# Performance work log

Measured on AMD Instinct MI355X. Metric: run time of the kernel, lower is better.

Reference implementation:

```python
import jax, jax.numpy as jnp
import numpy as np

N = 50000   # num_node
E = 1600000 # edge_size (N * avg_degree 32)
B = 64      # batch, hardcoded via repeat(64,1,1) in the torch module


def setup_inputs() -> dict:
    key = jax.random.key(0)
    k = jax.random.split(key, 8)
    return {
        "t": jax.random.normal(k[0], (1,), dtype=jnp.float32),
        "input": jax.random.normal(k[1], (B, N), dtype=jnp.float32),
        "edge_i": jax.random.randint(k[2], (E,), 0, N, dtype=jnp.int32),
        "edge_j": jax.random.randint(k[3], (E,), 0, N, dtype=jnp.int32),
        "weight_react": jax.random.normal(k[4], (1, E), dtype=jnp.float32) / 10.0,
        "weight_diff": jax.random.normal(k[5], (1, E), dtype=jnp.float32) / 1000.0,
        "bias_reaction": jax.random.normal(k[6], (1, N), dtype=jnp.float32) / 10.0,
        "bias_diffusion": jax.random.normal(k[7], (1, N), dtype=jnp.float32) / 10.0,
    }


def _lap_matvec(x, w, src, dst, n):
    # W[src_e, dst_e] = w_e (duplicates coalesce by sum, as torch sparse_coo_tensor does)
    # L = diag(colsum(W)) - W ; returns x @ L^T applied batched: out[b, v] = (L x[b])[v]
    col = jax.ops.segment_sum(w, dst, num_segments=n)                 # [N] column sums
    msg = jax.ops.segment_sum(w[:, None] * x[:, dst].T, src,
                              num_segments=n)                          # [N, B]
    return col[None, :] * x - msg.T                                   # [B, N]


def reference(t, input, edge_i, edge_j, weight_react, weight_diff,
              bias_reaction, bias_diffusion):
    x = input                                                          # [B, N]
    n = x.shape[1]
    # reaction Laplacian uses edges (i -> j); diffusion uses transposed (j -> i)
    reaction = _lap_matvec(x, weight_react[0], edge_i, edge_j, n) + bias_reaction
    diffusion = _lap_matvec(x, weight_diff[0], edge_j, edge_i, n) + bias_diffusion
    # up and down both True: tanh(reaction) + diffusion + input
    return jnp.tanh(reaction) + diffusion + x
```

## Files before the change

kernel.cpp:

```cpp
#include <hip/hip_runtime.h>
#include <hip/hip_fp16.h>


#define BKT_SHIFT 7
#define BKT_NODES 128
#define RCAP 4608
#define RCAP2 4992
#define CH 4096
#define NBP 512

#define RFL(x) __builtin_amdgcn_readfirstlane(x)

__device__ __forceinline__ unsigned bf16_rne(float f) {
    unsigned u = __float_as_uint(f);
    unsigned rb = (u >> 16) & 1u;
    u += 0x7FFFu + rb;
    return u >> 16;
}
__device__ __forceinline__ float bf16_lo(int y) {
    return __uint_as_float(((unsigned)y) << 16);
}
__device__ __forceinline__ float bf16_hi(int y) {
    return __uint_as_float((unsigned)y & 0xFFFF0000u);
}

__global__ void transpose_kernel(const float* __restrict__ x, __half* __restrict__ xth,
                                 int* __restrict__ gcur, int ngcur, int N) {
    __shared__ float tile[64][65];
    int v0 = blockIdx.x * 64;
    int tx = threadIdx.x;
    int ty = threadIdx.y;
    int flat = blockIdx.x * 1024 + ty * 64 + tx;
    if (flat < ngcur) gcur[flat] = 0;
    if (v0 + tx < N) {
        for (int b = ty; b < 64; b += 16)
            tile[tx][b] = x[b * N + v0 + tx];
    }
    __syncthreads();
    for (int vl = ty; vl < 64; vl += 16) {
        int v = v0 + vl;
        if (v < N)
            xth[(size_t)v * 64 + tx] = __float2half(tile[vl][tx]);
    }
}

__global__ void __launch_bounds__(512) partition_kernel(
        const int* __restrict__ ei, const int* __restrict__ ej,
        const float* __restrict__ wr, const float* __restrict__ wd,
        int* __restrict__ gcur, int2* __restrict__ runs,
        int E, int NB) {
    __shared__ int cnt[2 * NBP];
    __shared__ int base_a[2 * NBP];
    __shared__ int gb[2 * NBP];
    __shared__ int2 buf[2 * CH];

    int tid = threadIdx.x;
    int e0 = blockIdx.x * CH;
    int ch_len = min(CH, E - e0);
    if (ch_len <= 0) return;

    int my_i[8], my_j[8];
    unsigned my_w[8];
    #pragma unroll
    for (int k = 0; k < 8; ++k) {
        int t = tid + k * 512;
        if (t < ch_len) {
            int e = e0 + t;
            my_i[k] = ei[e];
            my_j[k] = ej[e];
            my_w[k] = (bf16_rne(wr[e]) << 16) | bf16_rne(wd[e]);
        } else {
            my_i[k] = -1;
        }
    }

    for (int b = tid; b < 2 * NBP; b += 512) cnt[b] = 0;
    __syncthreads();
    #pragma unroll
    for (int k = 0; k < 8; ++k) {
        if (my_i[k] >= 0) {
            atomicAdd(&cnt[my_i[k] >> BKT_SHIFT], 1);
            atomicAdd(&cnt[NBP + (my_j[k] >> BKT_SHIFT)], 1);
        }
    }
    __syncthreads();
    if (tid < 64) {
        int carry = 0;
        #pragma unroll
        for (int c = 0; c < (2 * NBP) / 64; ++c) {
            int idx = c * 64 + tid;
            int val = cnt[idx];
            int scan = val;
            for (int off = 1; off < 64; off <<= 1) {
                int n = __shfl_up(scan, off, 64);
                if (tid >= off) scan += n;
            }
            int excl = scan - val + carry;
            base_a[idx] = excl;
            cnt[idx] = excl;
            carry += __shfl(scan, 63, 64);
        }
    }
    __syncthreads();
    #pragma unroll
    for (int k = 0; k < 8; ++k) {
        if (my_i[k] >= 0) {
            int i = my_i[k], j = my_j[k];
            unsigned wv = my_w[k];
            int b0 = i >> BKT_SHIFT;
            int p0 = atomicAdd(&cnt[b0], 1);
            buf[p0] = make_int2((int)(((unsigned)b0 << 23) | ((unsigned)(i & 127) << 16) | (unsigned)j),
                                (int)wv);
            int b1 = j >> BKT_SHIFT;
            int p1 = atomicAdd(&cnt[NBP + b1], 1);
            buf[p1] = make_int2((int)(((unsigned)b1 << 23) | ((unsigned)(j & 127) << 16) | (unsigned)i),
                                (int)((wv << 16) | (wv >> 16)));
        }
    }
    __syncthreads();
    for (int cb = tid; cb < 2 * NBP; cb += 512) {
        int n = cnt[cb] - base_a[cb];
        if (n > 0) {
            int side = cb >> 9;
            int bkt = cb & (NBP - 1);
            gb[cb] = atomicAdd(&gcur[side * NB + bkt], n);
        }
    }
    __syncthreads();
    int total = 2 * ch_len;
    for (int t = tid; t < total; t += 512) {
        int2 p = buf[t];
        int side = (t >= ch_len) ? 1 : 0;
        int bkt = ((unsigned)p.x >> 23) & 0x1FF;
        int cb = side * NBP + bkt;
        int rank = gb[cb] + (t - base_a[cb]);
        if (rank < RCAP)
            runs[((size_t)(side * NB + bkt)) * RCAP + rank] = p;
    }
}

__global__ void __launch_bounds__(512) sortgather_kernel(
        const int* __restrict__ gcur, const int2* __restrict__ runs,
        const __half* __restrict__ xth,
        __half* __restrict__ msg, float* __restrict__ colsum,
        int NB, int N) {
    __shared__ int cnt[BKT_NODES];
    __shared__ int cur[BKT_NODES];
    __shared__ int pb[BKT_NODES];
    __shared__ float csum[BKT_NODES];
    __shared__ int src_c[RCAP];
    __shared__ unsigned char dlb[RCAP];
    __shared__ int dst[RCAP2];

    int sb = blockIdx.x;
    int side = (sb >= NB) ? 1 : 0;
    int b = sb - side * NB;
    int v0 = b << BKT_SHIFT;
    int len = min(gcur[sb], RCAP);
    size_t roff = (size_t)sb * RCAP;
    int tid = threadIdx.x;

    if (tid < BKT_NODES) { cnt[tid] = 0; csum[tid] = 0.f; }
    __syncthreads();
    for (int k = tid; k < len; k += 512) {
        int2 p = runs[roff + k];
        int dl = ((unsigned)p.x >> 16) & 0x7F;
        src_c[k] = (int)(((unsigned)p.y & 0xFFFF0000u) | ((unsigned)p.x & 0xFFFFu));
        dlb[k] = (unsigned char)dl;
        atomicAdd(&cnt[dl], 1);
        atomicAdd(&csum[dl], bf16_lo(p.y));
    }
    __syncthreads();
    if (tid < 64) {
        int carry = 0;
        #pragma unroll
        for (int c = 0; c < BKT_NODES / 64; ++c) {
            int idx = c * 64 + tid;
            int val = (cnt[idx] + 3) & ~3;
            int scan = val;
            for (int off = 1; off < 64; off <<= 1) {
                int n = __shfl_up(scan, off, 64);
                if (tid >= off) scan += n;
            }
            int excl = scan - val + carry;
            pb[idx] = excl;
            cur[idx] = excl;
            carry += __shfl(scan, 63, 64);
        }
    }
    __syncthreads();
    if (tid < BKT_NODES) {
        int pc = (cnt[tid] + 3) & ~3;
        for (int t = cnt[tid]; t < pc; ++t) dst[pb[tid] + t] = 0;
    }
    __syncthreads();
    for (int k = tid; k < len; k += 512) {
        int dl = dlb[k];
        int pos = atomicAdd(&cur[dl], 1);
        dst[pos] = src_c[k];
    }
    __syncthreads();

    int lane = tid & 63;
    int wid = tid >> 6;
    for (int t = 0; t < BKT_NODES / 8; ++t) {
        int dl = wid * (BKT_NODES / 8) + t;
        int v = v0 + dl;
        if (v >= N) continue;
        int base = pb[dl];
        int n = cnt[dl];
        int nq = (n + 3) >> 2;
        const int4* quads = (const int4*)(dst + base);
        float acc = 0.f;
        int q = 0;
        for (; q + 2 <= nq; q += 2) {
            int4 qa = quads[q];
            int4 qb = quads[q + 1];
            int p0 = RFL(qa.x), p1 = RFL(qa.y), p2 = RFL(qa.z), p3 = RFL(qa.w);
            int p4 = RFL(qb.x), p5 = RFL(qb.y), p6 = RFL(qb.z), p7 = RFL(qb.w);
            float x0 = __half2float(xth[((size_t)(p0 & 0xFFFF) << 6) + lane]);
            float x1 = __half2float(xth[((size_t)(p1 & 0xFFFF) << 6) + lane]);
            float x2 = __half2float(xth[((size_t)(p2 & 0xFFFF) << 6) + lane]);
            float x3 = __half2float(xth[((size_t)(p3 & 0xFFFF) << 6) + lane]);
            float x4 = __half2float(xth[((size_t)(p4 & 0xFFFF) << 6) + lane]);
            float x5 = __half2float(xth[((size_t)(p5 & 0xFFFF) << 6) + lane]);
            float x6 = __half2float(xth[((size_t)(p6 & 0xFFFF) << 6) + lane]);
            float x7 = __half2float(xth[((size_t)(p7 & 0xFFFF) << 6) + lane]);
            acc = fmaf(bf16_hi(p0), x0, acc);
            acc = fmaf(bf16_hi(p1), x1, acc);
            acc = fmaf(bf16_hi(p2), x2, acc);
            acc = fmaf(bf16_hi(p3), x3, acc);
            acc = fmaf(bf16_hi(p4), x4, acc);
            acc = fmaf(bf16_hi(p5), x5, acc);
            acc = fmaf(bf16_hi(p6), x6, acc);
            acc = fmaf(bf16_hi(p7), x7, acc);
        }
        if (q < nq) {
            int4 qa = quads[q];
            int p0 = RFL(qa.x), p1 = RFL(qa.y), p2 = RFL(qa.z), p3 = RFL(qa.w);
            float x0 = __half2float(xth[((size_t)(p0 & 0xFFFF) << 6) + lane]);
            float x1 = __half2float(xth[((size_t)(p1 & 0xFFFF) << 6) + lane]);
            float x2 = __half2float(xth[((size_t)(p2 & 0xFFFF) << 6) + lane]);
            float x3 = __half2float(xth[((size_t)(p3 & 0xFFFF) << 6) + lane]);
            acc = fmaf(bf16_hi(p0), x0, acc);
            acc = fmaf(bf16_hi(p1), x1, acc);
            acc = fmaf(bf16_hi(p2), x2, acc);
            acc = fmaf(bf16_hi(p3), x3, acc);
        }
        msg[((size_t)side * N + v) * 64 + lane] = __float2half(acc);
        if (lane == 0)
            colsum[(size_t)side * N + v] = csum[dl];
    }
}

__global__ void final_kernel(const float* __restrict__ x,
                             const __half* __restrict__ msg,
                             const float* __restrict__ colsum,
                             const float* __restrict__ br, const float* __restrict__ bd,
                             float* __restrict__ out, int N) {
    __shared__ float tr[64][65];
    __shared__ float td[64][65];
    int v0 = blockIdx.x * 64;
    int tx = threadIdx.x;
    int ty = threadIdx.y;
    for (int vl = ty; vl < 64; vl += 16) {
        int v = v0 + vl;
        if (v < N) {
            tr[vl][tx] = __half2float(msg[(size_t)v * 64 + tx]);
            td[vl][tx] = __half2float(msg[((size_t)N + v) * 64 + tx]);
        }
    }
    __syncthreads();
    int v = v0 + tx;
    if (v < N) {
        float cold = colsum[v];
        float colr = colsum[(size_t)N + v];
        float brv = br[v], bdv = bd[v];
        for (int b = ty; b < 64; b += 16) {
            float xv = x[b * N + v];
            float r = colr * xv - tr[tx][b] + brv;
            float d = cold * xv - td[tx][b] + bdv;
            out[b * N + v] = tanhf(r) + d + xv;
        }
    }
}

extern "C" void kernel_launch(void* const* d_in, const int* in_sizes, int n_in,
                              void* d_out, int out_size, void* d_ws, size_t ws_size,
                              hipStream_t stream) {
    const float* x  = (const float*)d_in[1];
    const int*   ei = (const int*)d_in[2];
    const int*   ej = (const int*)d_in[3];
    const float* wr = (const float*)d_in[4];
    const float* wd = (const float*)d_in[5];
    const float* br = (const float*)d_in[6];
    const float* bd = (const float*)d_in[7];
    float* out = (float*)d_out;

    int E = in_sizes[2];
    int N = in_sizes[6];
    int NB = (N + BKT_NODES - 1) >> BKT_SHIFT;
    (void)out_size; (void)ws_size; (void)n_in;

    char* w = (char*)d_ws;
    __half* xth = (__half*)w;    w += (size_t)N * 64 * 2;
    __half* msg = (__half*)w;    w += (size_t)2 * N * 64 * 2;
    float* colsum = (float*)w;   w += (size_t)2 * N * 4;
    int* gcur   = (int*)w;       w += (size_t)2 * NB * 4;
    w = (char*)(((uintptr_t)w + 15) & ~(uintptr_t)15);
    int2* runs  = (int2*)w;

    dim3 tb(64, 16);
    int ntiles = (N + 63) / 64;
    transpose_kernel<<<ntiles, tb, 0, stream>>>(x, xth, gcur, 2 * NB, N);

    int nchunks = (E + CH - 1) / CH;
    partition_kernel<<<nchunks, 512, 0, stream>>>(ei, ej, wr, wd, gcur, runs, E, NB);

    sortgather_kernel<<<2 * NB, 512, 0, stream>>>(gcur, runs, xth, msg, colsum, NB, N);

    final_kernel<<<ntiles, tb, 0, stream>>>(x, msg, colsum, br, bd, out, N);
}
```

Before: 229.7 us.

## Split half-precision x into two 32-batch planes and gather two edges per wavefront

The transposed half-precision input is stored as two planes of 32 batch columns instead of one 64-wide row per node. The gather kernel makes two passes, one per plane. In each pass the two half-waves handle alternate edges and are combined with a cross-lane shuffle, so each gathered row is 64 bytes and the per-pass working set is halved for cache locality. Both partition and sortgather are also raised to 1024 threads per block, which may affect occupancy and adds an extra block barrier per pass.

```diff
diff --git a/kernel.cpp b/kernel.cpp
--- a/kernel.cpp
+++ b/kernel.cpp
@@ -24,7 +24,7 @@
     return __uint_as_float((unsigned)y & 0xFFFF0000u);
 }
 
-__global__ void transpose_kernel(const float* __restrict__ x, __half* __restrict__ xth,
+__global__ void transpose_kernel(const float* __restrict__ x, __half* __restrict__ xh,
                                  int* __restrict__ gcur, int ngcur, int N) {
     __shared__ float tile[64][65];
     int v0 = blockIdx.x * 64;
@@ -37,14 +37,16 @@
             tile[tx][b] = x[b * N + v0 + tx];
     }
     __syncthreads();
+    int pass = tx >> 5;
+    int halfl = tx & 31;
     for (int vl = ty; vl < 64; vl += 16) {
         int v = v0 + vl;
         if (v < N)
-            xth[(size_t)v * 64 + tx] = __float2half(tile[vl][tx]);
-    }
-}
-
-__global__ void __launch_bounds__(512) partition_kernel(
+            xh[((size_t)pass * N + v) * 32 + halfl] = __float2half(tile[vl][tx]);
+    }
+}
+
+__global__ void __launch_bounds__(1024) partition_kernel(
         const int* __restrict__ ei, const int* __restrict__ ej,
         const float* __restrict__ wr, const float* __restrict__ wd,
         int* __restrict__ gcur, int2* __restrict__ runs,
@@ -59,11 +61,11 @@
     int ch_len = min(CH, E - e0);
     if (ch_len <= 0) return;
 
-    int my_i[8], my_j[8];
-    unsigned my_w[8];
+    int my_i[4], my_j[4];
+    unsigned my_w[4];
     #pragma unroll
-    for (int k = 0; k < 8; ++k) {
-        int t = tid + k * 512;
+    for (int k = 0; k < 4; ++k) {
+        int t = tid + k * 1024;
         if (t < ch_len) {
             int e = e0 + t;
             my_i[k] = ei[e];
@@ -74,10 +76,10 @@
         }
     }
 
-    for (int b = tid; b < 2 * NBP; b += 512) cnt[b] = 0;
+    if (tid < 2 * NBP) cnt[tid] = 0;
     __syncthreads();
     #pragma unroll
-    for (int k = 0; k < 8; ++k) {
+    for (int k = 0; k < 4; ++k) {
         if (my_i[k] >= 0) {
             atomicAdd(&cnt[my_i[k] >> BKT_SHIFT], 1);
             atomicAdd(&cnt[NBP + (my_j[k] >> BKT_SHIFT)], 1);
@@ -103,7 +105,7 @@
     }
     __syncthreads();
     #pragma unroll
-    for (int k = 0; k < 8; ++k) {
+    for (int k = 0; k < 4; ++k) {
         if (my_i[k] >= 0) {
             int i = my_i[k], j = my_j[k];
             unsigned wv = my_w[k];
@@ -118,17 +120,17 @@
         }
     }
     __syncthreads();
-    for (int cb = tid; cb < 2 * NBP; cb += 512) {
-        int n = cnt[cb] - base_a[cb];
+    if (tid < 2 * NBP) {
+        int n = cnt[tid] - base_a[tid];
         if (n > 0) {
-            int side = cb >> 9;
-            int bkt = cb & (NBP - 1);
-            gb[cb] = atomicAdd(&gcur[side * NB + bkt], n);
+            int side = tid >> 9;
+            int bkt = tid & (NBP - 1);
+            gb[tid] = atomicAdd(&gcur[side * NB + bkt], n);
         }
     }
     __syncthreads();
     int total = 2 * ch_len;
-    for (int t = tid; t < total; t += 512) {
+    for (int t = tid; t < total; t += 1024) {
         int2 p = buf[t];
         int side = (t >= ch_len) ? 1 : 0;
         int bkt = ((unsigned)p.x >> 23) & 0x1FF;
@@ -139,9 +141,17 @@
     }
 }
 
-__global__ void __launch_bounds__(512) sortgather_kernel(
+__device__ __forceinline__ void pair_acc(int pA, int pB, const __half* __restrict__ xp,
+                                         int halfl, bool hi, float& acc) {
+    int o = hi ? (pB & 0xFFFF) : (pA & 0xFFFF);
+    float w = hi ? bf16_hi(pB) : bf16_hi(pA);
+    float xv = __half2float(xp[((size_t)o << 5) + halfl]);
+    acc = fmaf(w, xv, acc);
+}
+
+__global__ void __launch_bounds__(1024) sortgather_kernel(
         const int* __restrict__ gcur, const int2* __restrict__ runs,
-        const __half* __restrict__ xth,
+        const __half* __restrict__ xh,
         __half* __restrict__ msg, float* __restrict__ colsum,
         int NB, int N) {
     __shared__ int cnt[BKT_NODES];
@@ -162,7 +172,7 @@
 
     if (tid < BKT_NODES) { cnt[tid] = 0; csum[tid] = 0.f; }
     __syncthreads();
-    for (int k = tid; k < len; k += 512) {
+    for (int k = tid; k < len; k += 1024) {
         int2 p = runs[roff + k];
         int dl = ((unsigned)p.x >> 16) & 0x7F;
         src_c[k] = (int)(((unsigned)p.y & 0xFFFF0000u) | ((unsigned)p.x & 0xFFFFu));
@@ -194,7 +204,7 @@
         for (int t = cnt[tid]; t < pc; ++t) dst[pb[tid] + t] = 0;
     }
     __syncthreads();
-    for (int k = tid; k < len; k += 512) {
+    for (int k = tid; k < len; k += 1024) {
         int dl = dlb[k];
         int pos = atomicAdd(&cur[dl], 1);
         dst[pos] = src_c[k];
@@ -202,54 +212,43 @@
     __syncthreads();
 
     int lane = tid & 63;
+    int halfl = lane & 31;
+    bool hi = lane >= 32;
     int wid = tid >> 6;
-    for (int t = 0; t < BKT_NODES / 8; ++t) {
-        int dl = wid * (BKT_NODES / 8) + t;
-        int v = v0 + dl;
-        if (v >= N) continue;
-        int base = pb[dl];
-        int n = cnt[dl];
-        int nq = (n + 3) >> 2;
-        const int4* quads = (const int4*)(dst + base);
-        float acc = 0.f;
-        int q = 0;
-        for (; q + 2 <= nq; q += 2) {
-            int4 qa = quads[q];
-            int4 qb = quads[q + 1];
-            int p0 = RFL(qa.x), p1 = RFL(qa.y), p2 = RFL(qa.z), p3 = RFL(qa.w);
-            int p4 = RFL(qb.x), p5 = RFL(qb.y), p6 = RFL(qb.z), p7 = RFL(qb.w);
-            float x0 = __half2float(xth[((size_t)(p0 & 0xFFFF) << 6) + lane]);
-            float x1 = __half2float(xth[((size_t)(p1 & 0xFFFF) << 6) + lane]);
-            float x2 = __half2float(xth[((size_t)(p2 & 0xFFFF) << 6) + lane]);
-            float x3 = __half2float(xth[((size_t)(p3 & 0xFFFF) << 6) + lane]);
-            float x4 = __half2float(xth[((size_t)(p4 & 0xFFFF) << 6) + lane]);
-            float x5 = __half2float(xth[((size_t)(p5 & 0xFFFF) << 6) + lane]);
-            float x6 = __half2float(xth[((size_t)(p6 & 0xFFFF) << 6) + lane]);
-            float x7 = __half2float(xth[((size_t)(p7 & 0xFFFF) << 6) + lane]);
-            acc = fmaf(bf16_hi(p0), x0, acc);
-            acc = fmaf(bf16_hi(p1), x1, acc);
-            acc = fmaf(bf16_hi(p2), x2, acc);
-            acc = fmaf(bf16_hi(p3), x3, acc);
-            acc = fmaf(bf16_hi(p4), x4, acc);
-            acc = fmaf(bf16_hi(p5), x5, acc);
-            acc = fmaf(bf16_hi(p6), x6, acc);
-            acc = fmaf(bf16_hi(p7), x7, acc);
-        }
-        if (q < nq) {
-            int4 qa = quads[q];
-            int p0 = RFL(qa.x), p1 = RFL(qa.y), p2 = RFL(qa.z), p3 = RFL(qa.w);
-            float x0 = __half2float(xth[((size_t)(p0 & 0xFFFF) << 6) + lane]);
-            float x1 = __half2float(xth[((size_t)(p1 & 0xFFFF) << 6) + lane]);
-            float x2 = __half2float(xth[((size_t)(p2 & 0xFFFF) << 6) + lane]);
-            float x3 = __half2float(xth[((size_t)(p3 & 0xFFFF) << 6) + lane]);
-            acc = fmaf(bf16_hi(p0), x0, acc);
-            acc = fmaf(bf16_hi(p1), x1, acc);
-            acc = fmaf(bf16_hi(p2), x2, acc);
-            acc = fmaf(bf16_hi(p3), x3, acc);
-        }
-        msg[((size_t)side * N + v) * 64 + lane] = __float2half(acc);
-        if (lane == 0)
-            colsum[(size_t)side * N + v] = csum[dl];
+    for (int pass = 0; pass < 2; ++pass) {
+        const __half* xp = xh + (size_t)pass * N * 32;
+        for (int t = 0; t < BKT_NODES / 16; ++t) {
+            int dl = wid * (BKT_NODES / 16) + t;
+            int v = v0 + dl;
+            if (v >= N) continue;
+            int base = pb[dl];
+            int nq = (cnt[dl] + 3) >> 2;
+            const int4* quads = (const int4*)(dst + base);
+            float acc = 0.f;
+            int q = 0;
+            for (; q + 2 <= nq; q += 2) {
+                int4 qa = quads[q];
+                int4 qb = quads[q + 1];
+                int p0 = RFL(qa.x), p1 = RFL(qa.y), p2 = RFL(qa.z), p3 = RFL(qa.w);
+                int p4 = RFL(qb.x), p5 = RFL(qb.y), p6 = RFL(qb.z), p7 = RFL(qb.w);
+                pair_acc(p0, p1, xp, halfl, hi, acc);
+                pair_acc(p2, p3, xp, halfl, hi, acc);
+                pair_acc(p4, p5, xp, halfl, hi, acc);
+                pair_acc(p6, p7, xp, halfl, hi, acc);
+            }
+            if (q < nq) {
+                int4 qa = quads[q];
+                int p0 = RFL(qa.x), p1 = RFL(qa.y), p2 = RFL(qa.z), p3 = RFL(qa.w);
+                pair_acc(p0, p1, xp, halfl, hi, acc);
+                pair_acc(p2, p3, xp, halfl, hi, acc);
+            }
+            acc += __shfl_xor(acc, 32);
+            if (!hi)
+                msg[((size_t)side * N + v) * 64 + pass * 32 + halfl] = __float2half(acc);
+            if (pass == 0 && lane == 0)
+                colsum[(size_t)side * N + v] = csum[dl];
+        }
+        __syncthreads();
     }
 }
 
@@ -303,7 +302,7 @@
     (void)out_size; (void)ws_size; (void)n_in;
 
     char* w = (char*)d_ws;
-    __half* xth = (__half*)w;    w += (size_t)N * 64 * 2;
+    __half* xh  = (__half*)w;    w += (size_t)2 * N * 32 * 2;
     __half* msg = (__half*)w;    w += (size_t)2 * N * 64 * 2;
     float* colsum = (float*)w;   w += (size_t)2 * N * 4;
     int* gcur   = (int*)w;       w += (size_t)2 * NB * 4;
@@ -312,12 +311,12 @@
 
     dim3 tb(64, 16);
     int ntiles = (N + 63) / 64;
-    transpose_kernel<<<ntiles, tb, 0, stream>>>(x, xth, gcur, 2 * NB, N);
+    transpose_kernel<<<ntiles, tb, 0, stream>>>(x, xh, gcur, 2 * NB, N);
 
     int nchunks = (E + CH - 1) / CH;
-    partition_kernel<<<nchunks, 512, 0, stream>>>(ei, ej, wr, wd, gcur, runs, E, NB);
-
-    sortgather_kernel<<<2 * NB, 512, 0, stream>>>(gcur, runs, xth, msg, colsum, NB, N);
+    partition_kernel<<<nchunks, 1024, 0, stream>>>(ei, ej, wr, wd, gcur, runs, E, NB);
+
+    sortgather_kernel<<<2 * NB, 1024, 0, stream>>>(gcur, runs, xh, msg, colsum, NB, N);
 
     final_kernel<<<ntiles, tb, 0, stream>>>(x, msg, colsum, br, bd, out, N);
 }
```

After: 247.2 us. 1.08x slower.
